# Kernel optimization log

Hardware: AMD Instinct MI355X
Metric: run time of the kernel (lower is better)

## Reference

```python
import jax, jax.numpy as jnp
import numpy as np

def setup_inputs() -> dict:
    key = jax.random.key(0)
    ks = jax.random.split(key, 8)
    E, D_IN, D_OUT = 250000, 256, 256
    NUM_CAMS, NUM_POINTS = 500, 100000
    return {
        "edge_features": jax.random.normal(ks[0], (E, D_IN), dtype=jnp.float32),
        "cam_indices": jax.random.randint(ks[1], (E,), 0, NUM_CAMS, dtype=jnp.int64 if jax.config.jax_enable_x64 else jnp.int32),
        "point_indices": jax.random.randint(ks[2], (E,), 0, NUM_POINTS, dtype=jnp.int64 if jax.config.jax_enable_x64 else jnp.int32),
        "num_cams": NUM_CAMS,
        "num_points": NUM_POINTS,
        "W_cam": jax.random.normal(ks[3], (D_OUT, D_IN), dtype=jnp.float32) / np.sqrt(D_IN),
        "W_point": jax.random.normal(ks[4], (D_OUT, D_IN), dtype=jnp.float32) / np.sqrt(D_IN),
        "W_attn": jax.random.normal(ks[5], (1, 2 * D_OUT), dtype=jnp.float32) / np.sqrt(2 * D_OUT),
        "W_final": jax.random.normal(ks[6], (D_OUT, 2 * D_OUT), dtype=jnp.float32) / np.sqrt(2 * D_OUT),
        "b_final": jax.random.normal(ks[7], (D_OUT,), dtype=jnp.float32) * 0.01,
    }

def reference(edge_features, cam_indices, point_indices, num_cams, num_points,
              W_cam, W_point, W_attn, W_final, b_final):
    # scatter-add aggregation per camera / per point node
    cam_agg = jax.ops.segment_sum(edge_features, cam_indices, num_segments=num_cams)      # [C, d_in]
    point_agg = jax.ops.segment_sum(edge_features, point_indices, num_segments=num_points)  # [P, d_in]
    # node projections (torch Linear: y = x @ W.T)
    h_cam = cam_agg @ W_cam.T        # [C, d_out]
    h_point = point_agg @ W_point.T  # [P, d_out]
    # gather back per edge and concat
    concat = jnp.concatenate([h_cam[cam_indices], h_point[point_indices]], axis=1)  # [E, 2*d_out]
    # attention score with GLOBAL softmax over all edges (dim=0)
    e = concat @ W_attn.T                       # [E, 1]
    attn = jax.nn.softmax(e, axis=0)            # [E, 1]
    new_features = (concat @ W_final.T + b_final) * attn  # [E, d_out]
    return jax.nn.relu(new_features)
```

## Files before the change

kernel.cpp:

```cpp
#include <hip/hip_runtime.h>
#include <hip/hip_bf16.h>
#include <math.h>

#define D 256
#define NCAM 500
#define NPT 100000
#define SCAN_NB ((NPT + 1023) / 1024)

typedef __attribute__((ext_vector_type(8))) short bf16x8;
typedef __attribute__((ext_vector_type(4))) float f32x4;

__device__ __forceinline__ unsigned short f2bf(float f) {
    unsigned u = __float_as_uint(f);
    u += 0x7FFFu + ((u >> 16) & 1u);
    return (unsigned short)(u >> 16);
}
__device__ __forceinline__ float bf2f(unsigned short h) {
    return __uint_as_float((unsigned)h << 16);
}

__global__ void hist_kernel(const int* __restrict__ ci, const int* __restrict__ pi,
                            int* __restrict__ cnt_pt, int* __restrict__ cnt_cam, int E) {
    int i = blockIdx.x * 256 + threadIdx.x;
    if (i < E) {
        atomicAdd(&cnt_pt[pi[i]], 1);
        atomicAdd(&cnt_cam[ci[i]], 1);
    }
}

__global__ __launch_bounds__(1024) void scan_partA(const int* __restrict__ cnt_pt,
                                                   int* __restrict__ blk_sum) {
    __shared__ int lds[1024];
    int t = threadIdx.x;
    int i = blockIdx.x * 1024 + t;
    lds[t] = (i < NPT) ? cnt_pt[i] : 0;
    __syncthreads();
    for (int s = 512; s > 0; s >>= 1) {
        if (t < s) lds[t] += lds[t + s];
        __syncthreads();
    }
    if (t == 0) blk_sum[blockIdx.x] = lds[0];
}

__global__ __launch_bounds__(512) void scan_partB(const int* __restrict__ blk_sum,
                                                  int* __restrict__ blk_base,
                                                  int* __restrict__ off_pt,
                                                  const int* __restrict__ cnt_cam,
                                                  int* __restrict__ off_cam,
                                                  int* __restrict__ cur_cam) {
    __shared__ int lds[512];
    int t = threadIdx.x;
    lds[t] = (t < SCAN_NB) ? blk_sum[t] : 0;
    __syncthreads();
    for (int off = 1; off < 512; off <<= 1) {
        int v = (t >= off) ? lds[t - off] : 0;
        __syncthreads();
        lds[t] += v;
        __syncthreads();
    }
    if (t < SCAN_NB) blk_base[t] = (t == 0) ? 0 : lds[t - 1];
    if (t == SCAN_NB) off_pt[NPT] = lds[SCAN_NB - 1];
    __syncthreads();
    lds[t] = (t < NCAM) ? cnt_cam[t] : 0;
    __syncthreads();
    for (int off = 1; off < 512; off <<= 1) {
        int v = (t >= off) ? lds[t - off] : 0;
        __syncthreads();
        lds[t] += v;
        __syncthreads();
    }
    if (t < NCAM) {
        int ex = (t == 0) ? 0 : lds[t - 1];
        off_cam[t] = ex;
        cur_cam[t] = ex;
    }
    if (t == NCAM) off_cam[NCAM] = lds[NCAM - 1];
}

__global__ __launch_bounds__(1024) void scan_partC(const int* __restrict__ cnt_pt,
                                                   const int* __restrict__ blk_base,
                                                   int* __restrict__ off_pt,
                                                   int* __restrict__ cur_pt) {
    __shared__ int lds[1024];
    int t = threadIdx.x;
    int i = blockIdx.x * 1024 + t;
    lds[t] = (i < NPT) ? cnt_pt[i] : 0;
    __syncthreads();
    for (int off = 1; off < 1024; off <<= 1) {
        int v = (t >= off) ? lds[t - off] : 0;
        __syncthreads();
        lds[t] += v;
        __syncthreads();
    }
    if (i < NPT) {
        int ex = blk_base[blockIdx.x] + ((t == 0) ? 0 : lds[t - 1]);
        off_pt[i] = ex;
        cur_pt[i] = ex;
    }
}

__global__ void bucket_kernel(const int* __restrict__ ci, const int* __restrict__ pi,
                              int* __restrict__ cur_pt, int* __restrict__ cur_cam,
                              int* __restrict__ order_pt, int* __restrict__ order_cam,
                              int E) {
    int i = blockIdx.x * 256 + threadIdx.x;
    if (i < E) {
        int pos = atomicAdd(&cur_pt[pi[i]], 1);
        order_pt[pos] = i;
        int pos2 = atomicAdd(&cur_cam[ci[i]], 1);
        order_cam[pos2] = i;
    }
}

__global__ void pt_agg_kernel(const float* __restrict__ ef,
                              const int* __restrict__ order_pt,
                              const int* __restrict__ off_pt,
                              const float* __restrict__ vpt,
                              unsigned short* __restrict__ Ahi,
                              unsigned short* __restrict__ Alo,
                              float* __restrict__ apt) {
    int wave = threadIdx.x >> 6;
    int lane = threadIdx.x & 63;
    int p = blockIdx.x * 4 + wave;
    if (p >= NPT) return;
    int j0 = off_pt[p], j1 = off_pt[p + 1];
    float4 acc = make_float4(0.f, 0.f, 0.f, 0.f);
    for (int j = j0; j < j1; j++) {
        int e = order_pt[j];
        float4 v = *(const float4*)(ef + (size_t)e * D + lane * 4);
        acc.x += v.x; acc.y += v.y; acc.z += v.z; acc.w += v.w;
    }
    ushort4 h, l;
    h.x = f2bf(acc.x); l.x = f2bf(acc.x - bf2f(h.x));
    h.y = f2bf(acc.y); l.y = f2bf(acc.y - bf2f(h.y));
    h.z = f2bf(acc.z); l.z = f2bf(acc.z - bf2f(h.z));
    h.w = f2bf(acc.w); l.w = f2bf(acc.w - bf2f(h.w));
    *(ushort4*)(Ahi + (size_t)p * D + lane * 4) = h;
    *(ushort4*)(Alo + (size_t)p * D + lane * 4) = l;
    float4 vv = *(const float4*)(vpt + lane * 4);
    float d = acc.x * vv.x + acc.y * vv.y + acc.z * vv.z + acc.w * vv.w;
    for (int off = 32; off > 0; off >>= 1) d += __shfl_down(d, off);
    if (lane == 0) apt[p] = d;
}

__global__ void cam_agg_kernel(const float* __restrict__ ef,
                               const int* __restrict__ order_cam,
                               const int* __restrict__ off_cam,
                               float* __restrict__ cam_agg) {
    int c = blockIdx.x;
    int q = blockIdx.y;
    int t = threadIdx.x;
    int j0 = off_cam[c], j1 = off_cam[c + 1];
    float acc = 0.f;
    for (int j = j0 + q; j < j1; j += 8) {
        int e = order_cam[j];
        acc += ef[(size_t)e * D + t];
    }
    atomicAdd(&cam_agg[(size_t)c * D + t], acc);
}

__global__ void combine_weights(const float* __restrict__ Wcam,
                                const float* __restrict__ Wpt,
                                const float* __restrict__ Wattn,
                                const float* __restrict__ Wfin,
                                float* __restrict__ CcamT,
                                unsigned short* __restrict__ Bhi,
                                unsigned short* __restrict__ Blo,
                                float* __restrict__ vcam,
                                float* __restrict__ vpt) {
    int b = blockIdx.x;
    int i = threadIdx.x;
    if (b < 256) {
        int o = b;
        float acc = 0.f;
        for (int j = 0; j < 256; j++) acc += Wfin[o * 512 + j] * Wcam[j * 256 + i];
        CcamT[i * 256 + o] = acc;
    } else if (b < 512) {
        int o = b - 256;
        float acc = 0.f;
        for (int j = 0; j < 256; j++) acc += Wfin[o * 512 + 256 + j] * Wpt[j * 256 + i];
        unsigned short h = f2bf(acc);
        Bhi[o * 256 + i] = h;
        Blo[o * 256 + i] = f2bf(acc - bf2f(h));
    } else if (b == 512) {
        float acc = 0.f;
        for (int j = 0; j < 256; j++) acc += Wattn[j] * Wcam[j * 256 + i];
        vcam[i] = acc;
    } else {
        float acc = 0.f;
        for (int j = 0; j < 256; j++) acc += Wattn[256 + j] * Wpt[j * 256 + i];
        vpt[i] = acc;
    }
}

__global__ void cam_proj(const float* __restrict__ cam_agg,
                         const float* __restrict__ CcamT,
                         const float* __restrict__ vcam,
                         float* __restrict__ gcam,
                         float* __restrict__ acam) {
    __shared__ float row[256];
    __shared__ float red[256];
    int c = blockIdx.x;
    int t = threadIdx.x;
    row[t] = cam_agg[(size_t)c * 256 + t];
    __syncthreads();
    float acc = 0.f;
    for (int i = 0; i < 256; i++) acc += row[i] * CcamT[i * 256 + t];
    gcam[(size_t)c * 256 + t] = acc;
    red[t] = row[t] * vcam[t];
    __syncthreads();
    for (int s = 128; s > 0; s >>= 1) {
        if (t < s) red[t] += red[t + s];
        __syncthreads();
    }
    if (t == 0) acam[c] = red[0];
}

__global__ __launch_bounds__(256) void gemm_mfma(const unsigned short* __restrict__ Ahi,
                                                 const unsigned short* __restrict__ Alo,
                                                 const unsigned short* __restrict__ Bhi,
                                                 const unsigned short* __restrict__ Blo,
                                                 float* __restrict__ Cout, int M) {
    int wave = threadIdx.x >> 6;
    int lane = threadIdx.x & 63;
    int m0 = blockIdx.x * 64;
    int n0 = wave * 64;
    int fr = lane & 15;
    int kg = (lane >> 4) * 8;
    f32x4 acc[4][4] = {};
    size_t ar[4];
#pragma unroll
    for (int f = 0; f < 4; f++) {
        int row = m0 + f * 16 + fr;
        if (row >= M) row = M - 1;
        ar[f] = (size_t)row * 256 + kg;
    }
    size_t brow = (size_t)(n0 + fr) * 256 + kg;
    for (int k0 = 0; k0 < 256; k0 += 32) {
        bf16x8 ah[4], al[4], bh[4], bl[4];
#pragma unroll
        for (int f = 0; f < 4; f++) {
            ah[f] = *(const bf16x8*)(Ahi + ar[f] + k0);
            al[f] = *(const bf16x8*)(Alo + ar[f] + k0);
            bh[f] = *(const bf16x8*)(Bhi + brow + (size_t)f * 16 * 256 + k0);
            bl[f] = *(const bf16x8*)(Blo + brow + (size_t)f * 16 * 256 + k0);
        }
#pragma unroll
        for (int mf = 0; mf < 4; mf++) {
#pragma unroll
            for (int nf = 0; nf < 4; nf++) {
                acc[mf][nf] = __builtin_amdgcn_mfma_f32_16x16x32_bf16(ah[mf], bh[nf], acc[mf][nf], 0, 0, 0);
                acc[mf][nf] = __builtin_amdgcn_mfma_f32_16x16x32_bf16(ah[mf], bl[nf], acc[mf][nf], 0, 0, 0);
                acc[mf][nf] = __builtin_amdgcn_mfma_f32_16x16x32_bf16(al[mf], bh[nf], acc[mf][nf], 0, 0, 0);
            }
        }
    }
    int rbase = (lane >> 4) * 4;
#pragma unroll
    for (int mf = 0; mf < 4; mf++) {
#pragma unroll
        for (int r = 0; r < 4; r++) {
            int row = m0 + mf * 16 + rbase + r;
            if (row < M) {
#pragma unroll
                for (int nf = 0; nf < 4; nf++)
                    Cout[(size_t)row * 256 + n0 + nf * 16 + fr] = acc[mf][nf][r];
            }
        }
    }
}

__device__ __forceinline__ unsigned float_key(float f) {
    unsigned b = __float_as_uint(f);
    return (b & 0x80000000u) ? ~b : (b | 0x80000000u);
}
__device__ __forceinline__ float key_float(unsigned k) {
    return __uint_as_float((k & 0x80000000u) ? (k & 0x7FFFFFFFu) : ~k);
}

__global__ void e_max_kernel(const int* __restrict__ ci, const int* __restrict__ pi,
                             const float* __restrict__ acam, const float* __restrict__ apt,
                             float* __restrict__ ebuf, unsigned* __restrict__ maxkey, int E) {
    int i = blockIdx.x * 256 + threadIdx.x;
    float e = -INFINITY;
    if (i < E) {
        e = acam[ci[i]] + apt[pi[i]];
        ebuf[i] = e;
    }
    __shared__ float red[256];
    int t = threadIdx.x;
    red[t] = e;
    __syncthreads();
    for (int s = 128; s > 0; s >>= 1) {
        if (t < s) red[t] = fmaxf(red[t], red[t + s]);
        __syncthreads();
    }
    if (t == 0) atomicMax(maxkey, float_key(red[0]));
}

__global__ void sumexp_kernel(float* __restrict__ ebuf,
                              const unsigned* __restrict__ maxkey,
                              float* __restrict__ sumexp, int E) {
    int i = blockIdx.x * 256 + threadIdx.x;
    float mx = key_float(*maxkey);
    float p = 0.f;
    if (i < E) {
        p = expf(ebuf[i] - mx);
        ebuf[i] = p;
    }
    __shared__ float red[256];
    int t = threadIdx.x;
    red[t] = p;
    __syncthreads();
    for (int s = 128; s > 0; s >>= 1) {
        if (t < s) red[t] += red[t + s];
        __syncthreads();
    }
    if (t == 0) atomicAdd(sumexp, red[0]);
}

__global__ __launch_bounds__(256) void out_kernel(const int* __restrict__ ci, const int* __restrict__ pi,
                           const float* __restrict__ gcam, const float* __restrict__ gpt,
                           const float* __restrict__ bfin, const float* __restrict__ ebuf,
                           const float* __restrict__ sumexp, float* __restrict__ out, int E) {
    int lane = threadIdx.x & 63;
    int wid = (blockIdx.x * 256 + threadIdx.x) >> 6;
    int nw = (gridDim.x * 256) >> 6;
    float inv = 1.0f / (*sumexp);
    float4 bb = *(const float4*)(bfin + lane * 4);
    for (int e = wid; e < E; e += nw) {
        float scale = ebuf[e] * inv;
        int c = ci[e];
        int p = pi[e];
        float4 gc = *(const float4*)(gcam + (size_t)c * 256 + lane * 4);
        float4 gp = *(const float4*)(gpt + (size_t)p * 256 + lane * 4);
        float4 v;
        v.x = fmaxf((gc.x + gp.x + bb.x) * scale, 0.f);
        v.y = fmaxf((gc.y + gp.y + bb.y) * scale, 0.f);
        v.z = fmaxf((gc.z + gp.z + bb.z) * scale, 0.f);
        v.w = fmaxf((gc.w + gp.w + bb.w) * scale, 0.f);
        *(float4*)(out + (size_t)e * 256 + lane * 4) = v;
    }
}

extern "C" void kernel_launch(void* const* d_in, const int* in_sizes, int n_in,
                              void* d_out, int out_size, void* d_ws, size_t ws_size,
                              hipStream_t stream) {
    const float* ef    = (const float*)d_in[0];
    const int*   ci    = (const int*)d_in[1];
    const int*   pi    = (const int*)d_in[2];
    const float* Wcam  = (const float*)d_in[5];
    const float* Wpt   = (const float*)d_in[6];
    const float* Wattn = (const float*)d_in[7];
    const float* Wfin  = (const float*)d_in[8];
    const float* bfin  = (const float*)d_in[9];
    float* out = (float*)d_out;
    int E = in_sizes[0] / D;

    float* ws = (float*)d_ws;
    float* cam_agg = ws;
    float* aregion = cam_agg + (size_t)NCAM * D;
    unsigned short* Ahi = (unsigned short*)aregion;
    unsigned short* Alo = Ahi + (size_t)NPT * D;
    float* CcamT   = aregion + (size_t)NPT * D;
    float* bregion = CcamT + 65536;
    unsigned short* Bhi = (unsigned short*)bregion;
    unsigned short* Blo = Bhi + 65536;
    float* vcam    = bregion + 65536;
    float* vpt     = vcam + 256;
    float* gcam    = vpt + 256;
    float* acam    = gcam + (size_t)NCAM * D;
    float* gpt     = acam + 512;
    float* apt     = gpt + (size_t)NPT * D;
    float* ebuf    = apt + NPT;
    unsigned* maxkey = (unsigned*)(ebuf + E);
    float* sumexp  = (float*)(maxkey + 1);

    int* ib        = (int*)gpt;
    int* cnt_pt    = ib;
    int* cnt_cam   = cnt_pt + NPT;
    int* off_pt    = cnt_cam + NCAM;
    int* off_cam   = off_pt + NPT + 1;
    int* cur_pt    = off_cam + NCAM + 1;
    int* cur_cam   = cur_pt + NPT;
    int* order_pt  = cur_cam + NCAM;
    int* order_cam = order_pt + E;
    int* blk_sum   = order_cam + E;
    int* blk_base  = blk_sum + SCAN_NB;

    hipMemsetAsync(cam_agg, 0, (size_t)NCAM * D * sizeof(float), stream);
    hipMemsetAsync(maxkey, 0, 2 * sizeof(unsigned), stream);
    hipMemsetAsync(cnt_pt, 0, (size_t)(NPT + NCAM) * sizeof(int), stream);

    int eb = (E + 255) / 256;
    hist_kernel<<<eb, 256, 0, stream>>>(ci, pi, cnt_pt, cnt_cam, E);
    combine_weights<<<514, 256, 0, stream>>>(Wcam, Wpt, Wattn, Wfin, CcamT, Bhi, Blo, vcam, vpt);
    scan_partA<<<SCAN_NB, 1024, 0, stream>>>(cnt_pt, blk_sum);
    scan_partB<<<1, 512, 0, stream>>>(blk_sum, blk_base, off_pt, cnt_cam, off_cam, cur_cam);
    scan_partC<<<SCAN_NB, 1024, 0, stream>>>(cnt_pt, blk_base, off_pt, cur_pt);
    bucket_kernel<<<eb, 256, 0, stream>>>(ci, pi, cur_pt, cur_cam, order_pt, order_cam, E);
    pt_agg_kernel<<<(NPT + 3) / 4, 256, 0, stream>>>(ef, order_pt, off_pt, vpt, Ahi, Alo, apt);
    cam_agg_kernel<<<dim3(NCAM, 8), 256, 0, stream>>>(ef, order_cam, off_cam, cam_agg);
    cam_proj<<<NCAM, 256, 0, stream>>>(cam_agg, CcamT, vcam, gcam, acam);
    gemm_mfma<<<(NPT + 63) / 64, 256, 0, stream>>>(Ahi, Alo, Bhi, Blo, gpt, NPT);
    e_max_kernel<<<eb, 256, 0, stream>>>(ci, pi, acam, apt, ebuf, maxkey, E);
    sumexp_kernel<<<eb, 256, 0, stream>>>(ebuf, maxkey, sumexp, E);
    out_kernel<<<2048, 256, 0, stream>>>(ci, pi, gcam, gpt, bfin, ebuf, sumexp, out, E);
}
```

Baseline: 983.2 us.

## Fuse point GEMM with output epilogue and use single-pass blockwise softmax

The point-projection GEMM now keeps its 64x256 result tile in shared memory. Each block then writes the final outputs for all edges belonging to its 64 points, walking the point-sorted edge order. This removes writing the full gpt matrix to global memory and gathering it back per edge. The softmax now computes per-block max and sum-of-exp in one pass, and a small single-block kernel combines them, replacing the atomic max and atomic sum passes. The cost is 64 KB of LDS per block, which limits occupancy, and output rows are written in point-bucket order rather than sequentially.

```diff
diff --git a/kernel.cpp b/kernel.cpp
--- a/kernel.cpp
+++ b/kernel.cpp
@@ -216,11 +216,83 @@
     if (t == 0) acam[c] = red[0];
 }
 
-__global__ __launch_bounds__(256) void gemm_mfma(const unsigned short* __restrict__ Ahi,
-                                                 const unsigned short* __restrict__ Alo,
-                                                 const unsigned short* __restrict__ Bhi,
-                                                 const unsigned short* __restrict__ Blo,
-                                                 float* __restrict__ Cout, int M) {
+__global__ void e_kernel(const int* __restrict__ ci, const int* __restrict__ pi,
+                         const float* __restrict__ acam, const float* __restrict__ apt,
+                         float* __restrict__ ebuf, float* __restrict__ bmax,
+                         float* __restrict__ bsum, int E) {
+    int i = blockIdx.x * 256 + threadIdx.x;
+    int t = threadIdx.x;
+    float e = -INFINITY;
+    if (i < E) {
+        e = acam[ci[i]] + apt[pi[i]];
+        ebuf[i] = e;
+    }
+    __shared__ float red[256];
+    red[t] = e;
+    __syncthreads();
+    for (int s = 128; s > 0; s >>= 1) {
+        if (t < s) red[t] = fmaxf(red[t], red[t + s]);
+        __syncthreads();
+    }
+    float bm = red[0];
+    __syncthreads();
+    float p = (i < E) ? __expf(e - bm) : 0.f;
+    red[t] = p;
+    __syncthreads();
+    for (int s = 128; s > 0; s >>= 1) {
+        if (t < s) red[t] += red[t + s];
+        __syncthreads();
+    }
+    if (t == 0) {
+        bmax[blockIdx.x] = bm;
+        bsum[blockIdx.x] = red[0];
+    }
+}
+
+__global__ __launch_bounds__(1024) void softmax_combine(const float* __restrict__ bmax,
+                                                        const float* __restrict__ bsum,
+                                                        float* __restrict__ gsm, int nb) {
+    __shared__ float rmax[1024];
+    __shared__ float rsum[1024];
+    int t = threadIdx.x;
+    float m = -INFINITY;
+    for (int i = t; i < nb; i += 1024) m = fmaxf(m, bmax[i]);
+    rmax[t] = m;
+    __syncthreads();
+    for (int s = 512; s > 0; s >>= 1) {
+        if (t < s) rmax[t] = fmaxf(rmax[t], rmax[t + s]);
+        __syncthreads();
+    }
+    float gm = rmax[0];
+    __syncthreads();
+    float s = 0.f;
+    for (int i = t; i < nb; i += 1024) s += bsum[i] * __expf(bmax[i] - gm);
+    rsum[t] = s;
+    __syncthreads();
+    for (int st = 512; st > 0; st >>= 1) {
+        if (t < st) rsum[t] += rsum[t + st];
+        __syncthreads();
+    }
+    if (t == 0) {
+        gsm[0] = gm;
+        gsm[1] = 1.0f / rsum[0];
+    }
+}
+
+__global__ __launch_bounds__(256) void gemm_out(const unsigned short* __restrict__ Ahi,
+                                                const unsigned short* __restrict__ Alo,
+                                                const unsigned short* __restrict__ Bhi,
+                                                const unsigned short* __restrict__ Blo,
+                                                const int* __restrict__ order_pt,
+                                                const int* __restrict__ off_pt,
+                                                const int* __restrict__ ci,
+                                                const int* __restrict__ pi,
+                                                const float* __restrict__ ebuf,
+                                                const float* __restrict__ gsm,
+                                                const float* __restrict__ gcam,
+                                                const float* __restrict__ bfin,
+                                                float* __restrict__ out, int M) {
+    __shared__ float tile[64][256];
     int wave = threadIdx.x >> 6;
     int lane = threadIdx.x & 63;
     int m0 = blockIdx.x * 64;
@@ -260,85 +332,30 @@
     for (int mf = 0; mf < 4; mf++) {
 #pragma unroll
         for (int r = 0; r < 4; r++) {
-            int row = m0 + mf * 16 + rbase + r;
-            if (row < M) {
-#pragma unroll
-                for (int nf = 0; nf < 4; nf++)
-                    Cout[(size_t)row * 256 + n0 + nf * 16 + fr] = acc[mf][nf][r];
-            }
+#pragma unroll
+            for (int nf = 0; nf < 4; nf++)
+                tile[mf * 16 + rbase + r][n0 + nf * 16 + fr] = acc[mf][nf][r];
         }
     }
-}
-
-__device__ __forceinline__ unsigned float_key(float f) {
-    unsigned b = __float_as_uint(f);
-    return (b & 0x80000000u) ? ~b : (b | 0x80000000u);
-}
-__device__ __forceinline__ float key_float(unsigned k) {
-    return __uint_as_float((k & 0x80000000u) ? (k & 0x7FFFFFFFu) : ~k);
-}
-
-__global__ void e_max_kernel(const int* __restrict__ ci, const int* __restrict__ pi,
-                             const float* __restrict__ acam, const float* __restrict__ apt,
-                             float* __restrict__ ebuf, unsigned* __restrict__ maxkey, int E) {
-    int i = blockIdx.x * 256 + threadIdx.x;
-    float e = -INFINITY;
-    if (i < E) {
-        e = acam[ci[i]] + apt[pi[i]];
-        ebuf[i] = e;
-    }
-    __shared__ float red[256];
-    int t = threadIdx.x;
-    red[t] = e;
-    __syncthreads();
-    for (int s = 128; s > 0; s >>= 1) {
-        if (t < s) red[t] = fmaxf(red[t], red[t + s]);
-        __syncthreads();
-    }
-    if (t == 0) atomicMax(maxkey, float_key(red[0]));
-}
-
-__global__ void sumexp_kernel(float* __restrict__ ebuf,
-                              const unsigned* __restrict__ maxkey,
-                              float* __restrict__ sumexp, int E) {
-    int i = blockIdx.x * 256 + threadIdx.x;
-    float mx = key_float(*maxkey);
-    float p = 0.f;
-    if (i < E) {
-        p = expf(ebuf[i] - mx);
-        ebuf[i] = p;
-    }
-    __shared__ float red[256];
-    int t = threadIdx.x;
-    red[t] = p;
-    __syncthreads();
-    for (int s = 128; s > 0; s >>= 1) {
-        if (t < s) red[t] += red[t + s];
-        __syncthreads();
-    }
-    if (t == 0) atomicAdd(sumexp, red[0]);
-}
-
-__global__ __launch_bounds__(256) void out_kernel(const int* __restrict__ ci, const int* __restrict__ pi,
-                           const float* __restrict__ gcam, const float* __restrict__ gpt,
-                           const float* __restrict__ bfin, const float* __restrict__ ebuf,
-                           const float* __restrict__ sumexp, float* __restrict__ out, int E) {
-    int lane = threadIdx.x & 63;
-    int wid = (blockIdx.x * 256 + threadIdx.x) >> 6;
-    int nw = (gridDim.x * 256) >> 6;
-    float inv = 1.0f / (*sumexp);
+    __syncthreads();
+    float gmax = gsm[0];
+    float ginv = gsm[1];
+    int hi = m0 + 64; if (hi > M) hi = M;
+    int j0 = off_pt[m0];
+    int j1 = off_pt[hi];
     float4 bb = *(const float4*)(bfin + lane * 4);
-    for (int e = wid; e < E; e += nw) {
-        float scale = ebuf[e] * inv;
+    for (int j = j0 + wave; j < j1; j += 4) {
+        int e = order_pt[j];
+        int lp = pi[e] - m0;
         int c = ci[e];
-        int p = pi[e];
+        float scale = __expf(ebuf[e] - gmax) * ginv;
+        float4 tv = *(const float4*)&tile[lp][lane * 4];
         float4 gc = *(const float4*)(gcam + (size_t)c * 256 + lane * 4);
-        float4 gp = *(const float4*)(gpt + (size_t)p * 256 + lane * 4);
         float4 v;
-        v.x = fmaxf((gc.x + gp.x + bb.x) * scale, 0.f);
-        v.y = fmaxf((gc.y + gp.y + bb.y) * scale, 0.f);
-        v.z = fmaxf((gc.z + gp.z + bb.z) * scale, 0.f);
-        v.w = fmaxf((gc.w + gp.w + bb.w) * scale, 0.f);
+        v.x = fmaxf((tv.x + gc.x + bb.x) * scale, 0.f);
+        v.y = fmaxf((tv.y + gc.y + bb.y) * scale, 0.f);
+        v.z = fmaxf((tv.z + gc.z + bb.z) * scale, 0.f);
+        v.w = fmaxf((tv.w + gc.w + bb.w) * scale, 0.f);
         *(float4*)(out + (size_t)e * 256 + lane * 4) = v;
     }
 }
@@ -356,6 +373,7 @@
     const float* bfin  = (const float*)d_in[9];
     float* out = (float*)d_out;
     int E = in_sizes[0] / D;
+    int eb = (E + 255) / 256;
 
     float* ws = (float*)d_ws;
     float* cam_agg = ws;
@@ -370,13 +388,13 @@
     float* vpt     = vcam + 256;
     float* gcam    = vpt + 256;
     float* acam    = gcam + (size_t)NCAM * D;
-    float* gpt     = acam + 512;
-    float* apt     = gpt + (size_t)NPT * D;
+    float* apt     = acam + 512;
     float* ebuf    = apt + NPT;
-    unsigned* maxkey = (unsigned*)(ebuf + E);
-    float* sumexp  = (float*)(maxkey + 1);
-
-    int* ib        = (int*)gpt;
+    float* gsm     = ebuf + E;
+    float* bmax    = gsm + 2;
+    float* bsum    = bmax + 1024;
+
+    int* ib        = (int*)(bsum + 1024);
     int* cnt_pt    = ib;
     int* cnt_cam   = cnt_pt + NPT;
     int* off_pt    = cnt_cam + NCAM;
@@ -389,10 +407,8 @@
     int* blk_base  = blk_sum + SCAN_NB;
 
     hipMemsetAsync(cam_agg, 0, (size_t)NCAM * D * sizeof(float), stream);
-    hipMemsetAsync(maxkey, 0, 2 * sizeof(unsigned), stream);
     hipMemsetAsync(cnt_pt, 0, (size_t)(NPT + NCAM) * sizeof(int), stream);
 
-    int eb = (E + 255) / 256;
     hist_kernel<<<eb, 256, 0, stream>>>(ci, pi, cnt_pt, cnt_cam, E);
     combine_weights<<<514, 256, 0, stream>>>(Wcam, Wpt, Wattn, Wfin, CcamT, Bhi, Blo, vcam, vpt);
     scan_partA<<<SCAN_NB, 1024, 0, stream>>>(cnt_pt, blk_sum);
@@ -402,8 +418,8 @@
     pt_agg_kernel<<<(NPT + 3) / 4, 256, 0, stream>>>(ef, order_pt, off_pt, vpt, Ahi, Alo, apt);
     cam_agg_kernel<<<dim3(NCAM, 8), 256, 0, stream>>>(ef, order_cam, off_cam, cam_agg);
     cam_proj<<<NCAM, 256, 0, stream>>>(cam_agg, CcamT, vcam, gcam, acam);
-    gemm_mfma<<<(NPT + 63) / 64, 256, 0, stream>>>(Ahi, Alo, Bhi, Blo, gpt, NPT);
-    e_max_kernel<<<eb, 256, 0, stream>>>(ci, pi, acam, apt, ebuf, maxkey, E);
-    sumexp_kernel<<<eb, 256, 0, stream>>>(ebuf, maxkey, sumexp, E);
-    out_kernel<<<2048, 256, 0, stream>>>(ci, pi, gcam, gpt, bfin, ebuf, sumexp, out, E);
-}
+    e_kernel<<<eb, 256, 0, stream>>>(ci, pi, acam, apt, ebuf, bmax, bsum, E);
+    softmax_combine<<<1, 1024, 0, stream>>>(bmax, bsum, gsm, eb);
+    gemm_out<<<(NPT + 63) / 64, 256, 0, stream>>>(Ahi, Alo, Bhi, Blo, order_pt, off_pt,
+                                                  ci, pi, ebuf, gsm, gcam, bfin, out, NPT);
+}
```

After: 980.0 us. No clear change (-0.3%).
